# Optimization experiments

Hardware: AMD Instinct MI355X
Metric: run time of the kernel (lower is better)

The kernel has to match this reference:

```python
import jax, jax.numpy as jnp
import numpy as np

N_CELLS, N_CLASSES, N_GENES, N_EDGES, HID = 100000, 50, 500, 600000, 8
NEG_SLOPE = 0.2  # GATv2Conv default negative_slope


def setup_inputs() -> dict:
    key = jax.random.key(0)
    ks = jax.random.split(key, 10)
    X = jax.random.normal(ks[0], (N_CELLS, N_GENES), jnp.float32)
    Mu = jax.random.normal(ks[1], (N_CLASSES, N_GENES), jnp.float32)
    # variances must be strictly positive
    Var = jax.random.uniform(ks[2], (N_CLASSES, N_GENES), jnp.float32) + 0.5
    W = 0.1 * jax.random.normal(ks[3], (N_CELLS, N_CLASSES), jnp.float32)
    S = 1.0 + 0.05 * jax.random.normal(ks[4], (N_CELLS, 1), jnp.float32)
    edge_index = jax.random.randint(ks[5], (2, N_EDGES), 0, N_CELLS, jnp.int32)
    sc = 1.0 / np.sqrt(N_GENES)
    lin_l_w = sc * jax.random.normal(ks[6], (HID, N_GENES), jnp.float32)
    lin_l_b = jnp.zeros((HID,), jnp.float32)
    lin_r_w = sc * jax.random.normal(ks[7], (HID, N_GENES), jnp.float32)
    lin_r_b = jnp.zeros((HID,), jnp.float32)
    att = jax.random.normal(ks[8], (HID,), jnp.float32) / np.sqrt(HID)
    return dict(X=X, Mu=Mu, Var=Var, W=W, S=S, edge_index=edge_index,
                lin_l_w=lin_l_w, lin_l_b=lin_l_b,
                lin_r_w=lin_r_w, lin_r_b=lin_r_b, att=att)


def _forward(X, Mu, Var, W, S, lin_l_w, lin_l_b, lin_r_w, lin_r_b, att, edge_index):
    N = X.shape[0]
    P = jax.nn.softmax(W, axis=1)  # [N, C]

    # Gaussian log-likelihood term.
    # F[n,c] = -0.5 * sum_g (X[n,g] - Mu[c,g]*S[n])^2 / Var[c,g]
    # Expanded into GEMMs (algebraically identical, avoids the [N,C,G] intermediate):
    invV = 1.0 / Var                          # [C, G]
    t1 = (X * X) @ invV.T                     # [N, C]  sum_g X^2/Var
    t2 = X @ (Mu * invV).T                    # [N, C]  sum_g X*Mu/Var
    t3 = jnp.sum(Mu * Mu * invV, axis=1)      # [C]     sum_g Mu^2/Var
    Fmat = -0.5 * (t1 - 2.0 * S * t2 + (S * S) * t3[None, :])  # [N, C]
    ll_prot = jnp.sum(P * Fmat) / N

    # GATv2 attention coefficients (heads=1, add_self_loops=False).
    gl = X @ lin_l_w.T + lin_l_b              # [N, HID]  lin_l (source side)
    gr = X @ lin_r_w.T + lin_r_b              # [N, HID]  lin_r (target side)
    src, dst = edge_index[0], edge_index[1]
    e = jax.nn.leaky_relu(gl[src] + gr[dst], NEG_SLOPE)  # [E, HID]
    score = e @ att                                       # [E]
    # segment softmax over destination nodes
    m = jax.ops.segment_max(score, dst, num_segments=N)
    ex = jnp.exp(score - m[dst])
    denom = jax.ops.segment_sum(ex, dst, num_segments=N)
    alpha = ex / denom[dst]                               # [E]

    ce_space = -jnp.sum(P[src] * alpha[:, None] * jnp.log(P[dst] + 1e-8)) / N
    return ll_prot, ce_space, P


def reference(X, Mu, Var, W, S, edge_index, lin_l_w, lin_l_b, lin_r_w, lin_r_b, att):
    return _forward(X, Mu, Var, W, S, lin_l_w, lin_l_b, lin_r_w, lin_r_b, att, edge_index)
```

## Files before the change

### kernel.cpp

```cpp
#include <hip/hip_runtime.h>
#include <math.h>

#define N_CELLS   100000
#define N_CLASSES 50
#define N_GENES   500
#define N_EDGES   600000
#define HID       8
#define NKT       8
#define NB_FUSED  1563
#define NB_CE     391
#define PROWS     56

typedef __attribute__((ext_vector_type(4))) float f32x4;
typedef __attribute__((ext_vector_type(8))) short bf16x8;
typedef __attribute__((ext_vector_type(8))) unsigned short u16x8;

static const size_t OFF_BF    = 0;
static const size_t OFF_T3    = 147456;
static const size_t OFF_GLR   = 147712;
static const size_t OFF_PB    = 6547712;
static const size_t OFF_LQ    = 17747712;
static const size_t OFF_DENOM = 28947712;
static const size_t OFF_NUMER = 29347712;
static const size_t OFF_LLP   = 29747712;
static const size_t OFF_CEP   = 29754112;
static const size_t OFF_TKT   = 29755904;

__device__ __forceinline__ ushort f2bf(float f) {
    union { float f; unsigned u; } v; v.f = f;
    unsigned r = v.u + 0x7fffu + ((v.u >> 16) & 1u);
    return (ushort)(r >> 16);
}
__device__ __forceinline__ float bf2f(ushort b) {
    union { unsigned u; float f; } v; v.u = ((unsigned)b) << 16; return v.f;
}
__device__ __forceinline__ unsigned cvt_pk_bf16(float lo, float hi) {
    unsigned r;
    asm("v_cvt_pk_bf16_f32 %0, %1, %2" : "=v"(r) : "v"(lo), "v"(hi));
    return r;
}
__device__ __forceinline__ void gload16(const void* g, void* l) {
    __builtin_amdgcn_global_load_lds(
        (const __attribute__((address_space(1))) unsigned int*)g,
        (__attribute__((address_space(3))) unsigned int*)l,
        16, 0, 0);
}

__global__ __launch_bounds__(256) void k_front(const float* __restrict__ Var,
                                               const float* __restrict__ Mu,
                                               const float* __restrict__ wl,
                                               const float* __restrict__ wr,
                                               const float* __restrict__ W,
                                               ushort* __restrict__ Bf,
                                               float* __restrict__ t3,
                                               float* __restrict__ P,
                                               ushort* __restrict__ Pb,
                                               ushort* __restrict__ LQ,
                                               unsigned* __restrict__ zeroed,
                                               unsigned* __restrict__ ticket) {
    if (blockIdx.x < 301) {
        int gid = blockIdx.x * 256 + threadIdx.x;
        for (int i = gid; i < 200000; i += 77056) zeroed[i] = 0u;
        if (gid == 0) *ticket = 0u;
    }
    if (blockIdx.x < 288) {
        int id = blockIdx.x * 256 + threadIdx.x;
        float v = 0.f;
        if (id < 65536) {
            int e    = id & 7;
            int lane = (id >> 3) & 63;
            int j    = (id >> 9) & 15;
            int kt   = id >> 13;
            int t    = j >> 1, ss = j & 1;
            int s    = kt * 2 + ss;
            int k    = s * 32 + ((lane >> 4) << 3) + e;
            int c    = (t & 3) * 16 + (lane & 15);
            if (k < N_GENES && c < N_CLASSES)
                v = (t < 4) ? 1.0f / Var[c * N_GENES + k]
                            : Mu[c * N_GENES + k] / Var[c * N_GENES + k];
        } else {
            int rem  = id - 65536;
            int e    = rem & 7;
            int lane = (rem >> 3) & 63;
            int s    = rem >> 9;
            int k    = s * 32 + ((lane >> 4) << 3) + e;
            int h    = lane & 15;
            if (k < N_GENES)
                v = (h < HID) ? wl[h * N_GENES + k] : wr[(h - HID) * N_GENES + k];
        }
        Bf[id] = f2bf(v);
    } else if (blockIdx.x < 301) {
        int c    = (blockIdx.x - 288) * 4 + (threadIdx.x >> 6);
        int lane = threadIdx.x & 63;
        if (c >= N_CLASSES) return;
        float s = 0.f;
        for (int g = lane; g < N_GENES; g += 64) {
            float m = Mu[c * N_GENES + g];
            s += m * m / Var[c * N_GENES + g];
        }
        #pragma unroll
        for (int off = 32; off; off >>= 1) s += __shfl_xor(s, off);
        if (lane == 0) t3[c] = s;
    } else {
        int wid  = (blockIdx.x - 301) * 4 + (threadIdx.x >> 6);
        int lane = threadIdx.x & 63;
        float w = (lane < N_CLASSES) ? W[(size_t)wid * N_CLASSES + lane] : -__builtin_inff();
        float m = w;
        #pragma unroll
        for (int off = 32; off; off >>= 1) m = fmaxf(m, __shfl_xor(m, off));
        float e = (lane < N_CLASSES) ? expf(w - m) : 0.f;
        float s = e;
        #pragma unroll
        for (int off = 32; off; off >>= 1) s += __shfl_xor(s, off);
        float p = e / s;
        if (lane < N_CLASSES) P[(size_t)wid * N_CLASSES + lane] = p;
        if (lane < PROWS) {
            Pb[(size_t)wid * PROWS + lane] = (lane < N_CLASSES) ? f2bf(p) : 0;
            LQ[(size_t)wid * PROWS + lane] = (lane < N_CLASSES) ? f2bf(logf(p + 1e-8f)) : 0;
        }
    }
}

__global__ __launch_bounds__(256, 2) void k_fused(const float* __restrict__ X,
                                                  const float* __restrict__ S,
                                                  const float* __restrict__ P,
                                                  const ushort* __restrict__ Bf,
                                                  const float* __restrict__ t3,
                                                  const float* __restrict__ bl,
                                                  const float* __restrict__ br,
                                                  ushort* __restrict__ glrb,
                                                  float* __restrict__ llp) {
    __shared__ float  ldsA[2][4][16][16][4];
    __shared__ ushort ldsB[2][20][64][8];
    __shared__ float  wsum[4];
    int tid  = threadIdx.x;
    int lane = tid & 63;
    int wv   = tid >> 6;
    int lhi  = lane >> 4;
    int slot = lane & 15;
    int rbase = blockIdx.x * 64 + wv * 16;
    const char* Xc  = (const char*)X;
    const char* Bfc = (const char*)Bf;

    int arow = rbase + slot;
    if (arow > N_CELLS - 1) arow = N_CELLS - 1;
    float m2s = -2.0f * S[arow];

    const f32x4 zz = {0.f, 0.f, 0.f, 0.f};
    f32x4 acc1[4], acc2[4], acc3;
    #pragma unroll
    for (int ct = 0; ct < 4; ++ct) { acc1[ct] = zz; acc2[ct] = zz; }
    acc3 = zz;

#define STAGE(KT, BUF) do {                                                        \
    _Pragma("unroll")                                                              \
    for (int i = 0; i < 4; ++i) {                                                  \
        int rloc = i * 4 + lhi;                                                    \
        int row  = rbase + rloc; if (row > N_CELLS - 1) row = N_CELLS - 1;         \
        int gi   = (KT) * 16 + (slot ^ (rloc & 7)); if (gi > 124) gi = 124;        \
        gload16(Xc + (size_t)row * 2000 + (size_t)gi * 16, &ldsA[BUF][wv][i * 4][0][0]); \
    }                                                                              \
    _Pragma("unroll")                                                              \
    for (int i = 0; i < 5; ++i) {                                                  \
        int j = wv * 5 + i;                                                        \
        size_t src;                                                                \
        if (j < 16)      src = (size_t)(KT) * 16384 + (size_t)j * 1024;            \
        else if (j < 18) src = 131072 + ((size_t)(KT) * 2 + (size_t)(j - 16)) * 1024; \
        else             src = (size_t)(KT) * 16384;                               \
        gload16(Bfc + src + (size_t)lane * 16, &ldsB[BUF][j][0][0]);               \
    }                                                                              \
} while (0)

    STAGE(0, 0);

    #pragma unroll
    for (int kt = 0; kt < NKT; ++kt) {
        const int cur = kt & 1;
        if (kt < NKT - 1) {
            STAGE(kt + 1, cur ^ 1);
            __builtin_amdgcn_sched_barrier(0);
            asm volatile("s_waitcnt vmcnt(9)" ::: "memory");
        } else {
            __builtin_amdgcn_sched_barrier(0);
            asm volatile("s_waitcnt vmcnt(0)" ::: "memory");
        }
        __builtin_amdgcn_sched_barrier(0);
        __builtin_amdgcn_s_barrier();
        __builtin_amdgcn_sched_barrier(0);

        const bf16x8* BL = (const bf16x8*)&ldsB[cur][0][0][0];
        #pragma unroll
        for (int ks = 0; ks < 2; ++ks) {
            int key = slot & 7;
            int c0  = ks * 8 + lhi * 2;
            f32x4 xa = *(const f32x4*)&ldsA[cur][wv][slot][c0 ^ key][0];
            f32x4 xb = *(const f32x4*)&ldsA[cur][wv][slot][(c0 + 1) ^ key][0];
            union { bf16x8 v; unsigned u[4]; } a1, a2;
            a1.u[0] = cvt_pk_bf16(xa[0] * xa[0], xa[1] * xa[1]);
            a1.u[1] = cvt_pk_bf16(xa[2] * xa[2], xa[3] * xa[3]);
            a1.u[2] = cvt_pk_bf16(xb[0] * xb[0], xb[1] * xb[1]);
            a1.u[3] = cvt_pk_bf16(xb[2] * xb[2], xb[3] * xb[3]);
            a2.u[0] = cvt_pk_bf16(m2s * xa[0], m2s * xa[1]);
            a2.u[1] = cvt_pk_bf16(m2s * xa[2], m2s * xa[3]);
            a2.u[2] = cvt_pk_bf16(m2s * xb[0], m2s * xb[1]);
            a2.u[3] = cvt_pk_bf16(m2s * xb[2], m2s * xb[3]);
            bf16x8 bg = BL[(16 + ks) * 64 + lane];
            #pragma unroll
            for (int ct = 0; ct < 4; ++ct)
                acc1[ct] = __builtin_amdgcn_mfma_f32_16x16x32_bf16(a1.v, BL[(ct * 2 + ks) * 64 + lane], acc1[ct], 0, 0, 0);
            #pragma unroll
            for (int ct = 0; ct < 4; ++ct)
                acc2[ct] = __builtin_amdgcn_mfma_f32_16x16x32_bf16(a2.v, BL[((4 + ct) * 2 + ks) * 64 + lane], acc2[ct], 0, 0, 0);
            acc3 = __builtin_amdgcn_mfma_f32_16x16x32_bf16(a2.v, bg, acc3, 0, 0, 0);
        }
        __builtin_amdgcn_sched_barrier(0);
        __builtin_amdgcn_s_barrier();
        __builtin_amdgcn_sched_barrier(0);
    }
#undef STAGE

    int col = lane & 15;
    int rg  = lane >> 4;
    float bias = (col < HID) ? bl[col] : br[col - HID];
    float part = 0.f;
    #pragma unroll
    for (int r = 0; r < 4; ++r) {
        int row = rbase + rg * 4 + r;
        if (row < N_CELLS) {
            float s2 = S[row];
            glrb[(size_t)row * 16 + col] = f2bf(acc3[r] / (-2.0f * s2) + bias);
            float ss = s2 * s2;
            #pragma unroll
            for (int ct = 0; ct < 4; ++ct) {
                int c = ct * 16 + col;
                if (c < N_CLASSES) {
                    float F = -0.5f * (acc1[ct][r] + acc2[ct][r] + ss * t3[c]);
                    part = fmaf(P[(size_t)row * N_CLASSES + c], F, part);
                }
            }
        }
    }
    #pragma unroll
    for (int off = 32; off; off >>= 1) part += __shfl_xor(part, off);
    if (lane == 0) wsum[wv] = part;
    __syncthreads();
    if (tid == 0) llp[blockIdx.x] = wsum[0] + wsum[1] + wsum[2] + wsum[3];
}

__global__ __launch_bounds__(256) void k_edge(const int* __restrict__ ei,
                                              const ushort* __restrict__ glrb,
                                              const float* __restrict__ att,
                                              const ushort* __restrict__ Pb,
                                              const ushort* __restrict__ LQ,
                                              float* __restrict__ denom,
                                              float* __restrict__ numer) {
    int e = blockIdx.x * 256 + threadIdx.x;
    if (e >= N_EDGES) return;
    int src = ei[e], dst = ei[N_EDGES + e];
    u16x8 gv = *(const u16x8*)(glrb + (size_t)src * 16);
    u16x8 hv = *(const u16x8*)(glrb + (size_t)dst * 16 + 8);
    const float4* at = (const float4*)att;
    float4 a0 = at[0], a1 = at[1];
    float t, s = 0.f;
    t = bf2f(gv[0]) + bf2f(hv[0]); t = t > 0.f ? t : 0.2f * t; s = fmaf(a0.x, t, s);
    t = bf2f(gv[1]) + bf2f(hv[1]); t = t > 0.f ? t : 0.2f * t; s = fmaf(a0.y, t, s);
    t = bf2f(gv[2]) + bf2f(hv[2]); t = t > 0.f ? t : 0.2f * t; s = fmaf(a0.z, t, s);
    t = bf2f(gv[3]) + bf2f(hv[3]); t = t > 0.f ? t : 0.2f * t; s = fmaf(a0.w, t, s);
    t = bf2f(gv[4]) + bf2f(hv[4]); t = t > 0.f ? t : 0.2f * t; s = fmaf(a1.x, t, s);
    t = bf2f(gv[5]) + bf2f(hv[5]); t = t > 0.f ? t : 0.2f * t; s = fmaf(a1.y, t, s);
    t = bf2f(gv[6]) + bf2f(hv[6]); t = t > 0.f ? t : 0.2f * t; s = fmaf(a1.z, t, s);
    t = bf2f(gv[7]) + bf2f(hv[7]); t = t > 0.f ? t : 0.2f * t; s = fmaf(a1.w, t, s);
    float ex = expf(s);

    const u16x8* ps = (const u16x8*)(Pb + (size_t)src * PROWS);
    const u16x8* ld = (const u16x8*)(LQ + (size_t)dst * PROWS);
    float v = 0.f;
    #pragma unroll
    for (int i = 0; i < 7; ++i) {
        u16x8 pv = ps[i], lv = ld[i];
        #pragma unroll
        for (int j = 0; j < 8; ++j)
            v = fmaf(bf2f(pv[j]), bf2f(lv[j]), v);
    }
    atomicAdd(denom + dst, ex);
    atomicAdd(numer + dst, ex * v);
}

__global__ __launch_bounds__(256) void k_ce_final(const float* __restrict__ denom,
                                                  const float* __restrict__ numer,
                                                  const float* __restrict__ llp,
                                                  float* __restrict__ cep,
                                                  unsigned* __restrict__ ticket,
                                                  float* __restrict__ out) {
    __shared__ float wsum[4];
    __shared__ unsigned lastv;
    __shared__ double l1[256], l2[256];
    int n = blockIdx.x * 256 + threadIdx.x;
    float v = 0.f;
    if (n < N_CELLS) {
        float d = denom[n];
        v = (d > 0.f) ? numer[n] / d : 0.f;
    }
    #pragma unroll
    for (int off = 32; off; off >>= 1) v += __shfl_xor(v, off);
    if ((threadIdx.x & 63) == 0) wsum[threadIdx.x >> 6] = v;
    __syncthreads();
    if (threadIdx.x == 0) {
        cep[blockIdx.x] = wsum[0] + wsum[1] + wsum[2] + wsum[3];
        __threadfence();
        lastv = atomicAdd(ticket, 1u);
    }
    __syncthreads();
    if (lastv == NB_CE - 1) {
        __threadfence();
        int t = threadIdx.x;
        double s1 = 0.0, s2 = 0.0;
        for (int i = t; i < NB_FUSED; i += 256) s1 += (double)llp[i];
        for (int i = t; i < NB_CE; i += 256) s2 += (double)cep[i];
        l1[t] = s1; l2[t] = s2;
        __syncthreads();
        for (int off = 128; off; off >>= 1) {
            if (t < off) { l1[t] += l1[t + off]; l2[t] += l2[t + off]; }
            __syncthreads();
        }
        if (t == 0) {
            out[0] = (float)(l1[0] / (double)N_CELLS);
            out[1] = (float)(-l2[0] / (double)N_CELLS);
        }
    }
}

extern "C" void kernel_launch(void* const* d_in, const int* in_sizes, int n_in,
                              void* d_out, int out_size, void* d_ws, size_t ws_size,
                              hipStream_t stream) {
    const float* X   = (const float*)d_in[0];
    const float* Mu  = (const float*)d_in[1];
    const float* Var = (const float*)d_in[2];
    const float* W   = (const float*)d_in[3];
    const float* S   = (const float*)d_in[4];
    const int*   ei  = (const int*)d_in[5];
    const float* wl  = (const float*)d_in[6];
    const float* bl  = (const float*)d_in[7];
    const float* wr  = (const float*)d_in[8];
    const float* br  = (const float*)d_in[9];
    const float* att = (const float*)d_in[10];
    float* out = (float*)d_out;
    char*  ws  = (char*)d_ws;

    ushort*   Bf    = (ushort*)(ws + OFF_BF);
    float*    t3    = (float*)(ws + OFF_T3);
    ushort*   glrb  = (ushort*)(ws + OFF_GLR);
    ushort*   Pb    = (ushort*)(ws + OFF_PB);
    ushort*   LQ    = (ushort*)(ws + OFF_LQ);
    float*    denom = (float*)(ws + OFF_DENOM);
    float*    numer = (float*)(ws + OFF_NUMER);
    float*    llp   = (float*)(ws + OFF_LLP);
    float*    cep   = (float*)(ws + OFF_CEP);
    unsigned* tkt   = (unsigned*)(ws + OFF_TKT);
    float*    P     = out + 2;

    k_front   <<<301 + 25000, 256, 0, stream>>>(Var, Mu, wl, wr, W, Bf, t3, P, Pb, LQ,
                                                (unsigned*)(ws + OFF_DENOM), tkt);
    k_fused   <<<NB_FUSED, 256, 0, stream>>>(X, S, P, Bf, t3, bl, br, glrb, llp);
    k_edge    <<<(N_EDGES + 255) / 256, 256, 0, stream>>>(ei, glrb, att, Pb, LQ, denom, numer);
    k_ce_final<<<NB_CE, 256, 0, stream>>>(denom, numer, llp, cep, tkt, out);
}
```

Measured before the change: 175.9 us.

## Fuse row softmax of W into the fused GEMM kernel prologue

```diff
diff --git a/kernel.cpp b/kernel.cpp
--- a/kernel.cpp
+++ b/kernel.cpp
@@ -50,21 +50,16 @@
                                                const float* __restrict__ Mu,
                                                const float* __restrict__ wl,
                                                const float* __restrict__ wr,
-                                               const float* __restrict__ W,
                                                ushort* __restrict__ Bf,
                                                float* __restrict__ t3,
-                                               float* __restrict__ P,
-                                               ushort* __restrict__ Pb,
-                                               ushort* __restrict__ LQ,
                                                unsigned* __restrict__ zeroed,
                                                unsigned* __restrict__ ticket) {
-    if (blockIdx.x < 301) {
-        int gid = blockIdx.x * 256 + threadIdx.x;
-        for (int i = gid; i < 200000; i += 77056) zeroed[i] = 0u;
-        if (gid == 0) *ticket = 0u;
-    }
+    int gid = blockIdx.x * 256 + threadIdx.x;
+    for (int i = gid; i < 200000; i += 77056) zeroed[i] = 0u;
+    if (gid == 0) *ticket = 0u;
+
     if (blockIdx.x < 288) {
-        int id = blockIdx.x * 256 + threadIdx.x;
+        int id = gid;
         float v = 0.f;
         if (id < 65536) {
             int e    = id & 7;
@@ -89,7 +84,7 @@
                 v = (h < HID) ? wl[h * N_GENES + k] : wr[(h - HID) * N_GENES + k];
         }
         Bf[id] = f2bf(v);
-    } else if (blockIdx.x < 301) {
+    } else {
         int c    = (blockIdx.x - 288) * 4 + (threadIdx.x >> 6);
         int lane = threadIdx.x & 63;
         if (c >= N_CLASSES) return;
@@ -101,34 +96,20 @@
         #pragma unroll
         for (int off = 32; off; off >>= 1) s += __shfl_xor(s, off);
         if (lane == 0) t3[c] = s;
-    } else {
-        int wid  = (blockIdx.x - 301) * 4 + (threadIdx.x >> 6);
-        int lane = threadIdx.x & 63;
-        float w = (lane < N_CLASSES) ? W[(size_t)wid * N_CLASSES + lane] : -__builtin_inff();
-        float m = w;
-        #pragma unroll
-        for (int off = 32; off; off >>= 1) m = fmaxf(m, __shfl_xor(m, off));
-        float e = (lane < N_CLASSES) ? expf(w - m) : 0.f;
-        float s = e;
-        #pragma unroll
-        for (int off = 32; off; off >>= 1) s += __shfl_xor(s, off);
-        float p = e / s;
-        if (lane < N_CLASSES) P[(size_t)wid * N_CLASSES + lane] = p;
-        if (lane < PROWS) {
-            Pb[(size_t)wid * PROWS + lane] = (lane < N_CLASSES) ? f2bf(p) : 0;
-            LQ[(size_t)wid * PROWS + lane] = (lane < N_CLASSES) ? f2bf(logf(p + 1e-8f)) : 0;
-        }
     }
 }
 
 __global__ __launch_bounds__(256, 2) void k_fused(const float* __restrict__ X,
                                                   const float* __restrict__ S,
-                                                  const float* __restrict__ P,
+                                                  const float* __restrict__ W,
                                                   const ushort* __restrict__ Bf,
                                                   const float* __restrict__ t3,
                                                   const float* __restrict__ bl,
                                                   const float* __restrict__ br,
                                                   ushort* __restrict__ glrb,
+                                                  float* __restrict__ P,
+                                                  ushort* __restrict__ Pb,
+                                                  ushort* __restrict__ LQ,
                                                   float* __restrict__ llp) {
     __shared__ float  ldsA[2][4][16][16][4];
     __shared__ ushort ldsB[2][20][64][8];
@@ -172,6 +153,44 @@
 } while (0)
 
     STAGE(0, 0);
+
+    {
+        const float* Wr = W + (size_t)arow * N_CLASSES + lhi;
+        float pv[13];
+        const int nj = (lhi < 2) ? 13 : 12;
+        float mx = -__builtin_inff();
+        #pragma unroll
+        for (int j = 0; j < 13; ++j)
+            if (j < nj) { pv[j] = Wr[4 * j]; mx = fmaxf(mx, pv[j]); }
+        mx = fmaxf(mx, __shfl_xor(mx, 16));
+        mx = fmaxf(mx, __shfl_xor(mx, 32));
+        float ssum = 0.f;
+        #pragma unroll
+        for (int j = 0; j < 13; ++j)
+            if (j < nj) { float e = expf(pv[j] - mx); pv[j] = e; ssum += e; }
+        ssum += __shfl_xor(ssum, 16);
+        ssum += __shfl_xor(ssum, 32);
+        float inv = 1.0f / ssum;
+        #pragma unroll
+        for (int j = 0; j < 13; ++j)
+            if (j < nj) {
+                int c = lhi + 4 * j;
+                float p = pv[j] * inv;
+                P [(size_t)arow * N_CLASSES + c] = p;
+                Pb[(size_t)arow * PROWS + c] = f2bf(p);
+                LQ[(size_t)arow * PROWS + c] = f2bf(logf(p + 1e-8f));
+            }
+        if (lhi == 0) {
+            #pragma unroll
+            for (int c = 50; c < 56; ++c) {
+                Pb[(size_t)arow * PROWS + c] = 0;
+                LQ[(size_t)arow * PROWS + c] = 0;
+            }
+        }
+    }
+    __builtin_amdgcn_sched_barrier(0);
+    asm volatile("s_waitcnt vmcnt(0)" ::: "memory");
+    __builtin_amdgcn_sched_barrier(0);
 
     #pragma unroll
     for (int kt = 0; kt < NKT; ++kt) {
@@ -235,7 +254,7 @@
                 int c = ct * 16 + col;
                 if (c < N_CLASSES) {
                     float F = -0.5f * (acc1[ct][r] + acc2[ct][r] + ss * t3[c]);
-                    part = fmaf(P[(size_t)row * N_CLASSES + c], F, part);
+                    part = fmaf(bf2f(Pb[(size_t)row * PROWS + c]), F, part);
                 }
             }
         }
@@ -359,9 +378,9 @@
     unsigned* tkt   = (unsigned*)(ws + OFF_TKT);
     float*    P     = out + 2;
 
-    k_front   <<<301 + 25000, 256, 0, stream>>>(Var, Mu, wl, wr, W, Bf, t3, P, Pb, LQ,
-                                                (unsigned*)(ws + OFF_DENOM), tkt);
-    k_fused   <<<NB_FUSED, 256, 0, stream>>>(X, S, P, Bf, t3, bl, br, glrb, llp);
+    k_front   <<<301, 256, 0, stream>>>(Var, Mu, wl, wr, Bf, t3,
+                                        (unsigned*)(ws + OFF_DENOM), tkt);
+    k_fused   <<<NB_FUSED, 256, 0, stream>>>(X, S, W, Bf, t3, bl, br, glrb, P, Pb, LQ, llp);
     k_edge    <<<(N_EDGES + 255) / 256, 256, 0, stream>>>(ei, glrb, att, Pb, LQ, denom, numer);
     k_ce_final<<<NB_CE, 256, 0, stream>>>(denom, numer, llp, cep, tkt, out);
 }
```

Result: slower. 183.8 us (+4.5%).
